# Kernel optimization log

Measured on AMD Instinct MI355X. Metric: run time of the kernel, lower is better.

## Reference

```python
import jax, jax.numpy as jnp
import numpy as np

EPS = 1e-5


def _bn(h, gamma, beta):
    # BatchNorm1d, training mode: biased batch statistics over nodes
    mu = jnp.mean(h, axis=0)
    var = jnp.mean(jnp.square(h - mu), axis=0)
    return (h - mu) * jax.lax.rsqrt(var + EPS) * gamma + beta


def setup_inputs() -> dict:
    key = jax.random.key(0)
    ks = jax.random.split(key, 12)
    N, E, D, H = 50000, 800000, 128, 256
    x = jax.random.normal(ks[0], (N, D), dtype=jnp.float32)
    edge_index = jax.random.randint(ks[1], (2, E), 0, N, dtype=jnp.int64)
    train_node_id = jax.random.randint(ks[2], (10000,), 0, N, dtype=jnp.int64)
    def lin(k, fan_in, fan_out):
        bound = 1.0 / np.sqrt(fan_in)
        return jax.random.uniform(k, (fan_in, fan_out), jnp.float32, -bound, bound)
    return {
        "x": x, "edge_index": edge_index, "train_node_id": train_node_id,
        "W1": lin(ks[3], D, H), "b1": jnp.zeros((H,), jnp.float32),
        "W2": lin(ks[4], H, H), "b2": jnp.zeros((H,), jnp.float32),
        "W3": lin(ks[5], H, H), "b3": jnp.zeros((H,), jnp.float32),
        "g1": jnp.ones((H,), jnp.float32), "be1": jnp.zeros((H,), jnp.float32),
        "g2": jnp.ones((H,), jnp.float32), "be2": jnp.zeros((H,), jnp.float32),
        "g3": jnp.ones((H,), jnp.float32), "be3": jnp.zeros((H,), jnp.float32),
        "Wl": lin(ks[6], H, H), "bl": jnp.zeros((H,), jnp.float32),
        "Wf": lin(ks[7], H, 1), "bf": jnp.zeros((1,), jnp.float32),
    }


def reference(x, edge_index, train_node_id, W1, b1, W2, b2, W3, b3,
              g1, be1, g2, be2, g3, be3, Wl, bl, Wf, bf):
    N = x.shape[0]
    loops = jnp.arange(N, dtype=edge_index.dtype)
    row = jnp.concatenate([edge_index[0], loops])  # destinations
    col = jnp.concatenate([edge_index[1], loops])  # sources
    deg = jax.ops.segment_sum(jnp.ones_like(row, dtype=x.dtype), row, num_segments=N)
    d_isqrt = jax.lax.rsqrt(deg)  # deg >= 1 due to self loops
    norm = (d_isqrt[row] * d_isqrt[col])[:, None]  # [E+N, 1]

    def gcn(h, W, b):
        hW = h @ W
        agg = jax.ops.segment_sum(hW[col] * norm, row, num_segments=N)
        return agg + b

    h = jax.nn.relu(_bn(gcn(x, W1, b1), g1, be1))
    h = jax.nn.relu(_bn(gcn(h, W2, b2), g2, be2))
    h = jax.nn.relu(_bn(gcn(h, W3, b3), g3, be3))
    h = jax.nn.relu(h @ Wl + bl)
    h = h[train_node_id]
    return jnp.squeeze(h @ Wf + bf, -1)
```

## Files before the change

### kernel.cpp

```cpp
#include <hip/hip_runtime.h>

typedef unsigned short u16;
typedef __attribute__((ext_vector_type(8))) short short8;
typedef __attribute__((ext_vector_type(4))) float f32x4;

#define CAP 96
#define GPB 25

#define DEVFN static __device__ __forceinline__

DEVFN float b2f(u16 u) {
    union { float f; unsigned v; } x; x.v = ((unsigned)u) << 16; return x.f;
}
DEVFN u16 f2b(float f) {
    union { float f; unsigned v; } x; x.f = f;
    unsigned r = x.v + 0x7fffu + ((x.v >> 16) & 1u);
    return (u16)(r >> 16);
}

DEVFN int detect64(const int* __restrict__ p) {
    int orv = 0;
#pragma unroll
    for (int i = 1; i < 64; i += 2) orv |= p[i];
    return (orv == 0) ? 1 : 0;
}

DEVFN void accum_row8(short8 v, float* acc) {
    const unsigned* u = (const unsigned*)&v;
#pragma unroll
    for (int k = 0; k < 4; k++) {
        union { float f; unsigned w; } lo, hi;
        lo.w = u[k] << 16;
        hi.w = u[k] & 0xffff0000u;
        acc[2 * k] += lo.f;
        acc[2 * k + 1] += hi.f;
    }
}

__global__ void k_init(const float* __restrict__ W1, const float* __restrict__ W2,
                       const float* __restrict__ W3, const float* __restrict__ Wl,
                       u16* __restrict__ T1, u16* __restrict__ T2,
                       u16* __restrict__ T3, u16* __restrict__ Tl,
                       int* __restrict__ ssrc, float* __restrict__ stat,
                       float* __restrict__ out, int N, int M) {
    int t = blockIdx.x * 256 + threadIdx.x;
    if (t < 229376) {
        const float* W; u16* T; int K; int idx;
        if (t < 32768)        { W = W1; T = T1; K = 128; idx = t; }
        else if (t < 98304)   { W = W2; T = T2; K = 256; idx = t - 32768; }
        else if (t < 163840)  { W = W3; T = T3; K = 256; idx = t - 98304; }
        else                  { W = Wl; T = Tl; K = 256; idx = t - 163840; }
        int k = idx >> 8, n = idx & 255;
        T[(size_t)n * K + k] = f2b(W[(size_t)k * 256 + n]);
    } else if (t < 229376 + 50000) {
        ssrc[(size_t)(t - 229376) * CAP] = 0;
    } else if (t < 229376 + 50000 + 1536) {
        stat[t - 229376 - 50000] = 0.0f;
    } else if (t < 229376 + 50000 + 1536 + 10000) {
        out[t - 229376 - 50000 - 1536] = 0.0f;
    }
}

__global__ void k_fillb(const int* __restrict__ ei, int* __restrict__ ssrc, int E) {
    int fl = detect64(ei);
    int t = blockIdx.x * 256 + threadIdx.x;
    int e0 = t * 2;
    if (e0 >= E) return;
    int r0, r1, c0, c1;
    bool two = (e0 + 1 < E);
    if (fl) {
        const int4* p4 = (const int4*)ei;
        int4 d = p4[t];
        int4 s = p4[(E >> 1) + t];
        r0 = d.x; r1 = d.z; c0 = s.x; c1 = s.z;
    } else {
        const int2* p2 = (const int2*)ei;
        int2 d = p2[t];
        int2 s = p2[(E >> 1) + t];
        r0 = d.x; r1 = d.y; c0 = s.x; c1 = s.y;
    }
    int p0 = atomicAdd(&ssrc[(size_t)r0 * CAP], 1);
    if (p0 < CAP - 1) ssrc[(size_t)r0 * CAP + 1 + p0] = c0;
    if (two) {
        int p1 = atomicAdd(&ssrc[(size_t)r1 * CAP], 1);
        if (p1 < CAP - 1) ssrc[(size_t)r1 * CAP + 1 + p1] = c1;
    }
}

__global__ void k_cvtx(const float* __restrict__ x, const int* __restrict__ ssrc,
                       float* __restrict__ disq, u16* __restrict__ xb, int n) {
    int i = (blockIdx.x * 256 + threadIdx.x) * 4;
    if (i >= n) return;
    int row = i >> 7;
    float d = rsqrtf((float)(ssrc[(size_t)row * CAP] + 1));
    if ((i & 127) == 0) disq[row] = d;
    float4 v = *(const float4*)(x + i);
    ushort4 o;
    o.x = f2b(v.x * d); o.y = f2b(v.y * d); o.z = f2b(v.z * d); o.w = f2b(v.w * d);
    *(ushort4*)(xb + i) = o;
}


template<int KS>
__global__ __launch_bounds__(256, 2) void k_gemm_rb(
        const u16* __restrict__ A, const u16* __restrict__ Wt,
        float* __restrict__ Cf, const int* __restrict__ idx,
        int Gtot, float* __restrict__ stat, const float* __restrict__ bias,
        const float* __restrict__ Wfp, const float* __restrict__ bfp,
        float* __restrict__ outp) {
    constexpr int K = KS * 32;
    __shared__ float sbuf[4][2][64];
    int wv = threadIdx.x >> 6;
    int lane = threadIdx.x & 63;
    int quad = lane >> 4;
    int mr = lane & 15;
    int colbase = blockIdx.y * 64;
    int g0 = blockIdx.x * GPB;

    short8 Bf[4][KS];
#pragma unroll
    for (int j = 0; j < 4; j++)
#pragma unroll
        for (int s = 0; s < KS; s++)
            Bf[j][s] = *(const short8*)(Wt + (size_t)(colbase + j * 16 + mr) * K + s * 32 + quad * 8);

    float4 bv4[4], wf4[4];
    if (Wfp) {
#pragma unroll
        for (int j = 0; j < 4; j++) {
            bv4[j] = *(const float4*)(bias + colbase + j * 16 + quad * 4);
            wf4[j] = *(const float4*)(Wfp + colbase + j * 16 + quad * 4);
        }
    }

    f32x4 sreg[4], s2reg[4];
#pragma unroll
    for (int j = 0; j < 4; j++) {
        sreg[j] = (f32x4){0.f, 0.f, 0.f, 0.f};
        s2reg[j] = (f32x4){0.f, 0.f, 0.f, 0.f};
    }
    int f = idx ? detect64(idx) : 0;

    for (int g = wv; g < GPB; g += 4) {
        int gg = g0 + g;
        if (gg >= Gtot) continue;
        int row = gg * 16 + mr;
        int arow = idx ? idx[(size_t)row << f] : row;
        const u16* Ap = A + (size_t)arow * K + quad * 8;

        short8 Af[KS];
#pragma unroll
        for (int s = 0; s < KS; s++) Af[s] = *(const short8*)(Ap + s * 32);

        f32x4 acc[4];
#pragma unroll
        for (int j = 0; j < 4; j++) acc[j] = (f32x4){0.f, 0.f, 0.f, 0.f};
#pragma unroll
        for (int s = 0; s < KS; s++)
#pragma unroll
            for (int j = 0; j < 4; j++)
                acc[j] = __builtin_amdgcn_mfma_f32_16x16x32_bf16(Bf[j][s], Af[s], acc[j], 0, 0, 0);

        if (Wfp) {
            float pr = 0.f;
#pragma unroll
            for (int j = 0; j < 4; j++) {
                const float* bj = (const float*)&bv4[j];
                const float* wj = (const float*)&wf4[j];
#pragma unroll
                for (int r = 0; r < 4; r++) {
                    float v = fmaxf(acc[j][r] + bj[r], 0.f);
                    pr += v * wj[r];
                }
            }
            pr += __shfl_xor(pr, 16, 64);
            pr += __shfl_xor(pr, 32, 64);
            if (quad == 0) {
                float v = pr;
                if (blockIdx.y == 0) v += bfp[0];
                atomicAdd(&outp[row], v);
            }
            continue;
        }

        float* cp = Cf + (size_t)row * 256 + colbase + quad * 4;
#pragma unroll
        for (int j = 0; j < 4; j++) {
            *(f32x4*)(cp + j * 16) = acc[j];
            sreg[j] += acc[j];
            s2reg[j] += acc[j] * acc[j];
        }
    }

    if (stat) {
#pragma unroll
        for (int j = 0; j < 4; j++) {
#pragma unroll
            for (int r = 0; r < 4; r++) {
                float a = sreg[j][r], b = s2reg[j][r];
                a += __shfl_xor(a, 1, 64); b += __shfl_xor(b, 1, 64);
                a += __shfl_xor(a, 2, 64); b += __shfl_xor(b, 2, 64);
                a += __shfl_xor(a, 4, 64); b += __shfl_xor(b, 4, 64);
                a += __shfl_xor(a, 8, 64); b += __shfl_xor(b, 8, 64);
                if (mr == 0) {
                    sbuf[wv][0][j * 16 + quad * 4 + r] = a;
                    sbuf[wv][1][j * 16 + quad * 4 + r] = b;
                }
            }
        }
        __syncthreads();
        int t = threadIdx.x;
        if (t < 128) {
            int which = t >> 6, c = t & 63;
            float v = sbuf[0][which][c] + sbuf[1][which][c] +
                      sbuf[2][which][c] + sbuf[3][which][c];
            atomicAdd(&stat[which * 256 + colbase + c], v);
        }
    }
}


__global__ __launch_bounds__(256) void k_gather256(
        const u16* __restrict__ src, const int* __restrict__ ssrc,
        const float* __restrict__ disq, u16* __restrict__ dst, int N) {
    int wave = threadIdx.x >> 6;
    int lane = threadIdx.x & 63;
    int half = lane >> 5;
    int l5 = lane & 31;
    int i = blockIdx.x * 4 + wave;
    if (i >= N) return;
    const u16* base = src + l5 * 8;
    const int* sp = ssrc + (size_t)i * CAP;
    float acc[8] = {0.f, 0.f, 0.f, 0.f, 0.f, 0.f, 0.f, 0.f};
    int e = min(sp[0], CAP - 1);
    int p = 0;
    for (; p + 8 <= e; p += 8) {
        int c0 = sp[1 + p + half];
        int c1 = sp[1 + p + 2 + half];
        int c2 = sp[1 + p + 4 + half];
        int c3 = sp[1 + p + 6 + half];
        short8 v0 = *(const short8*)(base + (size_t)c0 * 256);
        short8 v1 = *(const short8*)(base + (size_t)c1 * 256);
        short8 v2 = *(const short8*)(base + (size_t)c2 * 256);
        short8 v3 = *(const short8*)(base + (size_t)c3 * 256);
        accum_row8(v0, acc);
        accum_row8(v1, acc);
        accum_row8(v2, acc);
        accum_row8(v3, acc);
    }
    for (; p + 2 <= e; p += 2) {
        int c = sp[1 + p + half];
        short8 v = *(const short8*)(base + (size_t)c * 256);
        accum_row8(v, acc);
    }
    {
        int c = half ? i : ((p < e) ? sp[1 + p] : -1);
        if (c >= 0) {
            short8 v = *(const short8*)(base + (size_t)c * 256);
            accum_row8(v, acc);
        }
    }
#pragma unroll
    for (int k = 0; k < 8; k++) acc[k] += __shfl_xor(acc[k], 32, 64);
    if (half == 0) {
        float di = disq[i];
        short8 o;
        u16* op = (u16*)&o;
#pragma unroll
        for (int k = 0; k < 8; k++) op[k] = f2b(acc[k] * di);
        *(short8*)(dst + (size_t)i * 256 + l5 * 8) = o;
    }
}

__global__ __launch_bounds__(256) void k_gather128(
        const u16* __restrict__ src, const int* __restrict__ ssrc,
        const float* __restrict__ disq, u16* __restrict__ dst, int N) {
    int wave = threadIdx.x >> 6;
    int lane = threadIdx.x & 63;
    int q = lane >> 4;
    int l4 = lane & 15;
    int i = blockIdx.x * 4 + wave;
    if (i >= N) return;
    const u16* base = src + l4 * 8;
    const int* sp = ssrc + (size_t)i * CAP;
    float acc[8] = {0.f, 0.f, 0.f, 0.f, 0.f, 0.f, 0.f, 0.f};
    int e = min(sp[0], CAP - 1);
    int p = 0;
    for (; p + 8 <= e; p += 8) {
        int c0 = sp[1 + p + q];
        int c1 = sp[1 + p + 4 + q];
        short8 v0 = *(const short8*)(base + (size_t)c0 * 128);
        short8 v1 = *(const short8*)(base + (size_t)c1 * 128);
        accum_row8(v0, acc);
        accum_row8(v1, acc);
    }
    for (; p + 4 <= e; p += 4) {
        int c = sp[1 + p + q];
        short8 v = *(const short8*)(base + (size_t)c * 128);
        accum_row8(v, acc);
    }
    int rem = e - p;
    {
        int c = (q < rem) ? sp[1 + p + q] : ((q == 3) ? i : -1);
        if (c >= 0) {
            short8 v = *(const short8*)(base + (size_t)c * 128);
            accum_row8(v, acc);
        }
    }
#pragma unroll
    for (int k = 0; k < 8; k++) {
        acc[k] += __shfl_xor(acc[k], 16, 64);
        acc[k] += __shfl_xor(acc[k], 32, 64);
    }
    if (q == 0) {
        float di = disq[i];
        short8 o;
        u16* op = (u16*)&o;
#pragma unroll
        for (int k = 0; k < 8; k++) op[k] = f2b(acc[k] * di);
        *(short8*)(dst + (size_t)i * 128 + l4 * 8) = o;
    }
}


__global__ void k_bnapply(const float* __restrict__ t, const float* __restrict__ stat,
                          const float* __restrict__ gamma, const float* __restrict__ beta,
                          u16* __restrict__ h, int N, float invN,
                          const float* __restrict__ scale) {
    size_t tt = (size_t)blockIdx.x * 256 + threadIdx.x;
    size_t base = tt * 4;
    if (base >= (size_t)N * 256) return;
    int f0 = (int)(base & 255);
    float sc2 = scale ? scale[base >> 8] : 1.0f;
    float4 v = *(const float4*)(t + base);
    float r[4] = {v.x, v.y, v.z, v.w};
    ushort4 o;
    u16* op = (u16*)&o;
#pragma unroll
    for (int j = 0; j < 4; j++) {
        int f = f0 + j;
        float mean = stat[f] * invN;
        float var = stat[256 + f] * invN - mean * mean;
        float rstd = rsqrtf(var + 1e-5f);
        float sc = rstd * gamma[f];
        float sh = beta[f] - mean * sc;
        op[j] = f2b(fmaxf(r[j] * sc + sh, 0.0f) * sc2);
    }
    *(ushort4*)(h + base) = o;
}

__global__ void k_bnapply_idx(const float* __restrict__ t, const float* __restrict__ stat,
                              const float* __restrict__ gamma, const float* __restrict__ beta,
                              const int* __restrict__ idx, u16* __restrict__ zin,
                              int M, float invN) {
    int fl = detect64(idx);
    size_t tt = (size_t)blockIdx.x * 256 + threadIdx.x;
    size_t base = tt * 4;
    if (base >= (size_t)M * 256) return;
    int f0 = (int)(base & 255);
    int row = (int)(base >> 8);
    int node = idx[(size_t)row << fl];
    float4 v = *(const float4*)(t + (size_t)node * 256 + f0);
    float r[4] = {v.x, v.y, v.z, v.w};
    ushort4 o;
    u16* op = (u16*)&o;
#pragma unroll
    for (int j = 0; j < 4; j++) {
        int f = f0 + j;
        float mean = stat[f] * invN;
        float var = stat[256 + f] * invN - mean * mean;
        float rstd = rsqrtf(var + 1e-5f);
        float sc = rstd * gamma[f];
        float sh = beta[f] - mean * sc;
        op[j] = f2b(fmaxf(r[j] * sc + sh, 0.0f));
    }
    *(ushort4*)(zin + (size_t)row * 256 + f0) = o;
}


extern "C" void kernel_launch(void* const* d_in, const int* in_sizes, int n_in,
                              void* d_out, int out_size, void* d_ws, size_t ws_size,
                              hipStream_t stream) {
    const int D = 128, H = 256;
    const int N = in_sizes[0] / D;
    const int E = in_sizes[1] / 2;
    const int M = in_sizes[2];

    const float* x = (const float*)d_in[0];
    const int* ei = (const int*)d_in[1];
    const int* tnid = (const int*)d_in[2];
    const float* W1 = (const float*)d_in[3];
    const float* W2 = (const float*)d_in[5];
    const float* W3 = (const float*)d_in[7];
    const float* g1 = (const float*)d_in[9];
    const float* be1 = (const float*)d_in[10];
    const float* g2 = (const float*)d_in[11];
    const float* be2 = (const float*)d_in[12];
    const float* g3 = (const float*)d_in[13];
    const float* be3 = (const float*)d_in[14];
    const float* Wl = (const float*)d_in[15];
    const float* bl = (const float*)d_in[16];
    const float* Wf = (const float*)d_in[17];
    const float* bfp = (const float*)d_in[18];
    float* out = (float*)d_out;

    char* w = (char*)d_ws;
    size_t off = 0;
    auto carve = [&](size_t bytes) -> void* {
        void* p = w + off;
        off = (off + bytes + 255) & ~(size_t)255;
        return p;
    };

    float* stat = (float*)carve(3 * 512 * 4);
    float* disq = (float*)carve((size_t)N * 4);
    int* ssrc = (int*)carve((size_t)N * CAP * 4);
    u16* Wt1 = (u16*)carve((size_t)H * D * 2);
    u16* Wt2 = (u16*)carve((size_t)H * H * 2);
    u16* Wt3 = (u16*)carve((size_t)H * H * 2);
    u16* Wtl = (u16*)carve((size_t)H * H * 2);
    u16* xb = (u16*)carve((size_t)N * D * 2);
    u16* aggx = (u16*)carve((size_t)N * D * 2);
    u16* aggh = (u16*)carve((size_t)N * H * 2);
    float* tb = (float*)carve((size_t)N * H * 4);
    u16* hb = (u16*)carve((size_t)N * H * 2);
    u16* zin = (u16*)carve((size_t)M * H * 2);

    const float invN = 1.0f / (float)N;

    const int Gn = N / 16;
    const int Gm = M / 16;
    dim3 gemm_grid((Gn + GPB - 1) / GPB, 4);
    dim3 gemm_grid_m((Gm + GPB - 1) / GPB, 4);
    const int AB = (N + 3) / 4;
    const int PB = (int)(((size_t)N * H / 4 + 255) / 256);
    const int PBm = (int)(((size_t)M * H / 4 + 255) / 256);

    k_init<<<(229376 + 50000 + 1536 + 10000 + 255) / 256, 256, 0, stream>>>(
        W1, W2, W3, Wl, Wt1, Wt2, Wt3, Wtl, ssrc, stat, out, N, M);
    k_fillb<<<(E / 2 + 255) / 256, 256, 0, stream>>>(ei, ssrc, E);
    k_cvtx<<<(N * D / 4 + 255) / 256, 256, 0, stream>>>(x, ssrc, disq, xb, N * D);

    k_gather128<<<AB, 256, 0, stream>>>(xb, ssrc, disq, aggx, N);
    k_gemm_rb<4><<<gemm_grid, 256, 0, stream>>>(aggx, Wt1, tb, nullptr, Gn, stat, nullptr, nullptr, nullptr, nullptr);
    k_bnapply<<<PB, 256, 0, stream>>>(tb, stat, g1, be1, hb, N, invN, disq);
    k_gather256<<<AB, 256, 0, stream>>>(hb, ssrc, disq, aggh, N);
    k_gemm_rb<8><<<gemm_grid, 256, 0, stream>>>(aggh, Wt2, tb, nullptr, Gn, stat + 512, nullptr, nullptr, nullptr, nullptr);
    k_bnapply<<<PB, 256, 0, stream>>>(tb, stat + 512, g2, be2, hb, N, invN, disq);
    k_gather256<<<AB, 256, 0, stream>>>(hb, ssrc, disq, aggh, N);
    k_gemm_rb<8><<<gemm_grid, 256, 0, stream>>>(aggh, Wt3, tb, nullptr, Gn, stat + 1024, nullptr, nullptr, nullptr, nullptr);
    k_bnapply_idx<<<PBm, 256, 0, stream>>>(tb, stat + 1024, g3, be3, tnid, zin, M, invN);

    k_gemm_rb<8><<<gemm_grid_m, 256, 0, stream>>>(zin, Wtl, nullptr, nullptr, Gm, nullptr, bl, Wf, bfp, out);
}
```

Before: 447.8 us.

## Store features in 32-column planes and gather per plane with u16 adjacency

Feature matrices now use a planar layout of 32-column slabs, so each gather block works on one plane and touches a smaller, more cache-resident source slice. Adjacency is stored as 16-bit source ids in a fixed 32-slot array plus an overflow array, which shrinks the index footprint. The GEMMs read A through a plane stride, and the gather loops over the maximum degree among the 16 nodes handled by each wave. Risks: 16-bit ids only hold node indices below 65536, neighbours beyond 95 per node are silently dropped, and lanes whose node has a lower degree sit idle for the extra iterations.

```diff
diff --git a/kernel.cpp b/kernel.cpp
--- a/kernel.cpp
+++ b/kernel.cpp
@@ -4,7 +4,6 @@
 typedef __attribute__((ext_vector_type(8))) short short8;
 typedef __attribute__((ext_vector_type(4))) float f32x4;
 
-#define CAP 96
 #define GPB 25
 
 #define DEVFN static __device__ __forceinline__
@@ -41,7 +40,7 @@
                        const float* __restrict__ W3, const float* __restrict__ Wl,
                        u16* __restrict__ T1, u16* __restrict__ T2,
                        u16* __restrict__ T3, u16* __restrict__ Tl,
-                       int* __restrict__ ssrc, float* __restrict__ stat,
+                       int* __restrict__ cnt, float* __restrict__ stat,
                        float* __restrict__ out, int N, int M) {
     int t = blockIdx.x * 256 + threadIdx.x;
     if (t < 229376) {
@@ -52,16 +51,17 @@
         else                  { W = Wl; T = Tl; K = 256; idx = t - 163840; }
         int k = idx >> 8, n = idx & 255;
         T[(size_t)n * K + k] = f2b(W[(size_t)k * 256 + n]);
-    } else if (t < 229376 + 50000) {
-        ssrc[(size_t)(t - 229376) * CAP] = 0;
-    } else if (t < 229376 + 50000 + 1536) {
-        stat[t - 229376 - 50000] = 0.0f;
-    } else if (t < 229376 + 50000 + 1536 + 10000) {
-        out[t - 229376 - 50000 - 1536] = 0.0f;
-    }
-}
-
-__global__ void k_fillb(const int* __restrict__ ei, int* __restrict__ ssrc, int E) {
+    } else if (t < 229376 + N) {
+        cnt[t - 229376] = 0;
+    } else if (t < 229376 + N + 1536) {
+        stat[t - 229376 - N] = 0.0f;
+    } else if (t < 229376 + N + 1536 + M) {
+        out[t - 229376 - N - 1536] = 0.0f;
+    }
+}
+
+__global__ void k_fillb(const int* __restrict__ ei, int* __restrict__ cnt,
+                        u16* __restrict__ slots, u16* __restrict__ ovf, int E) {
     int fl = detect64(ei);
     int t = blockIdx.x * 256 + threadIdx.x;
     int e0 = t * 2;
@@ -79,33 +79,98 @@
         int2 s = p2[(E >> 1) + t];
         r0 = d.x; r1 = d.y; c0 = s.x; c1 = s.y;
     }
-    int p0 = atomicAdd(&ssrc[(size_t)r0 * CAP], 1);
-    if (p0 < CAP - 1) ssrc[(size_t)r0 * CAP + 1 + p0] = c0;
+    int p0 = atomicAdd(&cnt[r0], 1);
+    if (p0 < 32)      slots[(size_t)r0 * 32 + p0] = (u16)c0;
+    else if (p0 < 96) ovf[(size_t)r0 * 64 + (p0 - 32)] = (u16)c0;
     if (two) {
-        int p1 = atomicAdd(&ssrc[(size_t)r1 * CAP], 1);
-        if (p1 < CAP - 1) ssrc[(size_t)r1 * CAP + 1 + p1] = c1;
-    }
-}
-
-__global__ void k_cvtx(const float* __restrict__ x, const int* __restrict__ ssrc,
-                       float* __restrict__ disq, u16* __restrict__ xb, int n) {
-    int i = (blockIdx.x * 256 + threadIdx.x) * 4;
-    if (i >= n) return;
-    int row = i >> 7;
-    float d = rsqrtf((float)(ssrc[(size_t)row * CAP] + 1));
-    if ((i & 127) == 0) disq[row] = d;
-    float4 v = *(const float4*)(x + i);
+        int p1 = atomicAdd(&cnt[r1], 1);
+        if (p1 < 32)      slots[(size_t)r1 * 32 + p1] = (u16)c1;
+        else if (p1 < 96) ovf[(size_t)r1 * 64 + (p1 - 32)] = (u16)c1;
+    }
+}
+
+__global__ void k_cvtx(const float* __restrict__ x, const int* __restrict__ cnt,
+                       float* __restrict__ disq, u16* __restrict__ xb, int N) {
+    int t = blockIdx.x * 256 + threadIdx.x;
+    if (t >= N * 32) return;
+    int row = t >> 5;
+    int f0 = (t & 31) * 4;
+    float d = rsqrtf((float)(cnt[row] + 1));
+    if ((t & 31) == 0) disq[row] = d;
+    float4 v = *(const float4*)(x + (size_t)row * 128 + f0);
     ushort4 o;
     o.x = f2b(v.x * d); o.y = f2b(v.y * d); o.z = f2b(v.z * d); o.w = f2b(v.w * d);
-    *(ushort4*)(xb + i) = o;
+    *(ushort4*)(xb + (size_t)(f0 >> 5) * N * 32 + (size_t)row * 32 + (f0 & 31)) = o;
+}
+
+
+template<int PBITS>
+__global__ __launch_bounds__(256) void k_gatherP(
+        const u16* __restrict__ src, const int* __restrict__ cnt,
+        const u16* __restrict__ slots, const u16* __restrict__ ovf,
+        const float* __restrict__ disq, u16* __restrict__ dst, int N) {
+    const int NP = 1 << PBITS;
+    const size_t N32 = (size_t)N * 32;
+    int plane = blockIdx.x & (NP - 1);
+    int lane = threadIdx.x & 63;
+    int wv = threadIdx.x >> 6;
+    int j = lane >> 2;
+    int piece = lane & 3;
+    int d = (blockIdx.x >> PBITS) * 64 + wv * 16 + j;
+    bool live = d < N;
+    int e = live ? min(cnt[d], 95) : -1;
+
+    const u16* sbase = src + (size_t)plane * N32 + piece * 8;
+    const u16* sl = slots + (size_t)d * 32;
+    const u16* ov = ovf + (size_t)d * 64;
+
+    float acc[8] = {0.f, 0.f, 0.f, 0.f, 0.f, 0.f, 0.f, 0.f};
+
+    int m = e;
+    m = max(m, __shfl_xor(m, 4, 64));
+    m = max(m, __shfl_xor(m, 8, 64));
+    m = max(m, __shfl_xor(m, 16, 64));
+    m = max(m, __shfl_xor(m, 32, 64));
+
+    int mm = min(m, 31);
+#pragma unroll 4
+    for (int r = 0; r <= mm; r++) {
+        int c = -1;
+        if (r < e) c = (int)sl[r];
+        else if (r == e) c = d;
+        if (c >= 0) {
+            short8 v = *(const short8*)(sbase + (size_t)c * 32);
+            accum_row8(v, acc);
+        }
+    }
+    if (m >= 32) {
+        for (int r = 32; r <= m; r++) {
+            int c = -1;
+            if (r < e) c = (int)ov[r - 32];
+            else if (r == e) c = d;
+            if (c >= 0) {
+                short8 v = *(const short8*)(sbase + (size_t)c * 32);
+                accum_row8(v, acc);
+            }
+        }
+    }
+    if (live) {
+        float di = disq[d];
+        short8 o;
+        u16* op = (u16*)&o;
+#pragma unroll
+        for (int k = 0; k < 8; k++) op[k] = f2b(acc[k] * di);
+        __builtin_nontemporal_store(o,
+            (short8*)(dst + (size_t)plane * N32 + (size_t)d * 32 + piece * 8));
+    }
 }
 
 
 template<int KS>
 __global__ __launch_bounds__(256, 2) void k_gemm_rb(
         const u16* __restrict__ A, const u16* __restrict__ Wt,
-        float* __restrict__ Cf, const int* __restrict__ idx,
-        int Gtot, float* __restrict__ stat, const float* __restrict__ bias,
+        float* __restrict__ Cf, int PS, int Gtot,
+        float* __restrict__ stat, const float* __restrict__ bias,
         const float* __restrict__ Wfp, const float* __restrict__ bfp,
         float* __restrict__ outp) {
     constexpr int K = KS * 32;
@@ -139,18 +204,16 @@
         sreg[j] = (f32x4){0.f, 0.f, 0.f, 0.f};
         s2reg[j] = (f32x4){0.f, 0.f, 0.f, 0.f};
     }
-    int f = idx ? detect64(idx) : 0;
 
     for (int g = wv; g < GPB; g += 4) {
         int gg = g0 + g;
         if (gg >= Gtot) continue;
         int row = gg * 16 + mr;
-        int arow = idx ? idx[(size_t)row << f] : row;
-        const u16* Ap = A + (size_t)arow * K + quad * 8;
+        const u16* Ap = A + (size_t)row * 32 + quad * 8;
 
         short8 Af[KS];
 #pragma unroll
-        for (int s = 0; s < KS; s++) Af[s] = *(const short8*)(Ap + s * 32);
+        for (int s = 0; s < KS; s++) Af[s] = *(const short8*)(Ap + (size_t)s * PS);
 
         f32x4 acc[4];
 #pragma unroll
@@ -220,109 +283,6 @@
 }
 
 
-__global__ __launch_bounds__(256) void k_gather256(
-        const u16* __restrict__ src, const int* __restrict__ ssrc,
-        const float* __restrict__ disq, u16* __restrict__ dst, int N) {
-    int wave = threadIdx.x >> 6;
-    int lane = threadIdx.x & 63;
-    int half = lane >> 5;
-    int l5 = lane & 31;
-    int i = blockIdx.x * 4 + wave;
-    if (i >= N) return;
-    const u16* base = src + l5 * 8;
-    const int* sp = ssrc + (size_t)i * CAP;
-    float acc[8] = {0.f, 0.f, 0.f, 0.f, 0.f, 0.f, 0.f, 0.f};
-    int e = min(sp[0], CAP - 1);
-    int p = 0;
-    for (; p + 8 <= e; p += 8) {
-        int c0 = sp[1 + p + half];
-        int c1 = sp[1 + p + 2 + half];
-        int c2 = sp[1 + p + 4 + half];
-        int c3 = sp[1 + p + 6 + half];
-        short8 v0 = *(const short8*)(base + (size_t)c0 * 256);
-        short8 v1 = *(const short8*)(base + (size_t)c1 * 256);
-        short8 v2 = *(const short8*)(base + (size_t)c2 * 256);
-        short8 v3 = *(const short8*)(base + (size_t)c3 * 256);
-        accum_row8(v0, acc);
-        accum_row8(v1, acc);
-        accum_row8(v2, acc);
-        accum_row8(v3, acc);
-    }
-    for (; p + 2 <= e; p += 2) {
-        int c = sp[1 + p + half];
-        short8 v = *(const short8*)(base + (size_t)c * 256);
-        accum_row8(v, acc);
-    }
-    {
-        int c = half ? i : ((p < e) ? sp[1 + p] : -1);
-        if (c >= 0) {
-            short8 v = *(const short8*)(base + (size_t)c * 256);
-            accum_row8(v, acc);
-        }
-    }
-#pragma unroll
-    for (int k = 0; k < 8; k++) acc[k] += __shfl_xor(acc[k], 32, 64);
-    if (half == 0) {
-        float di = disq[i];
-        short8 o;
-        u16* op = (u16*)&o;
-#pragma unroll
-        for (int k = 0; k < 8; k++) op[k] = f2b(acc[k] * di);
-        *(short8*)(dst + (size_t)i * 256 + l5 * 8) = o;
-    }
-}
-
-__global__ __launch_bounds__(256) void k_gather128(
-        const u16* __restrict__ src, const int* __restrict__ ssrc,
-        const float* __restrict__ disq, u16* __restrict__ dst, int N) {
-    int wave = threadIdx.x >> 6;
-    int lane = threadIdx.x & 63;
-    int q = lane >> 4;
-    int l4 = lane & 15;
-    int i = blockIdx.x * 4 + wave;
-    if (i >= N) return;
-    const u16* base = src + l4 * 8;
-    const int* sp = ssrc + (size_t)i * CAP;
-    float acc[8] = {0.f, 0.f, 0.f, 0.f, 0.f, 0.f, 0.f, 0.f};
-    int e = min(sp[0], CAP - 1);
-    int p = 0;
-    for (; p + 8 <= e; p += 8) {
-        int c0 = sp[1 + p + q];
-        int c1 = sp[1 + p + 4 + q];
-        short8 v0 = *(const short8*)(base + (size_t)c0 * 128);
-        short8 v1 = *(const short8*)(base + (size_t)c1 * 128);
-        accum_row8(v0, acc);
-        accum_row8(v1, acc);
-    }
-    for (; p + 4 <= e; p += 4) {
-        int c = sp[1 + p + q];
-        short8 v = *(const short8*)(base + (size_t)c * 128);
-        accum_row8(v, acc);
-    }
-    int rem = e - p;
-    {
-        int c = (q < rem) ? sp[1 + p + q] : ((q == 3) ? i : -1);
-        if (c >= 0) {
-            short8 v = *(const short8*)(base + (size_t)c * 128);
-            accum_row8(v, acc);
-        }
-    }
-#pragma unroll
-    for (int k = 0; k < 8; k++) {
-        acc[k] += __shfl_xor(acc[k], 16, 64);
-        acc[k] += __shfl_xor(acc[k], 32, 64);
-    }
-    if (q == 0) {
-        float di = disq[i];
-        short8 o;
-        u16* op = (u16*)&o;
-#pragma unroll
-        for (int k = 0; k < 8; k++) op[k] = f2b(acc[k] * di);
-        *(short8*)(dst + (size_t)i * 128 + l4 * 8) = o;
-    }
-}
-
-
 __global__ void k_bnapply(const float* __restrict__ t, const float* __restrict__ stat,
                           const float* __restrict__ gamma, const float* __restrict__ beta,
                           u16* __restrict__ h, int N, float invN,
@@ -331,7 +291,8 @@
     size_t base = tt * 4;
     if (base >= (size_t)N * 256) return;
     int f0 = (int)(base & 255);
-    float sc2 = scale ? scale[base >> 8] : 1.0f;
+    int row = (int)(base >> 8);
+    float sc2 = scale ? scale[row] : 1.0f;
     float4 v = *(const float4*)(t + base);
     float r[4] = {v.x, v.y, v.z, v.w};
     ushort4 o;
@@ -346,7 +307,7 @@
         float sh = beta[f] - mean * sc;
         op[j] = f2b(fmaxf(r[j] * sc + sh, 0.0f) * sc2);
     }
-    *(ushort4*)(h + base) = o;
+    *(ushort4*)(h + (size_t)(f0 >> 5) * N * 32 + (size_t)row * 32 + (f0 & 31)) = o;
 }
 
 __global__ void k_bnapply_idx(const float* __restrict__ t, const float* __restrict__ stat,
@@ -374,7 +335,7 @@
         float sh = beta[f] - mean * sc;
         op[j] = f2b(fmaxf(r[j] * sc + sh, 0.0f));
     }
-    *(ushort4*)(zin + (size_t)row * 256 + f0) = o;
+    *(ushort4*)(zin + (size_t)(f0 >> 5) * M * 32 + (size_t)row * 32 + (f0 & 31)) = o;
 }
 
 
@@ -414,7 +375,9 @@
 
     float* stat = (float*)carve(3 * 512 * 4);
     float* disq = (float*)carve((size_t)N * 4);
-    int* ssrc = (int*)carve((size_t)N * CAP * 4);
+    int* cnt = (int*)carve((size_t)N * 4);
+    u16* slots = (u16*)carve((size_t)N * 32 * 2);
+    u16* ovf = (u16*)carve((size_t)N * 64 * 2);
     u16* Wt1 = (u16*)carve((size_t)H * D * 2);
     u16* Wt2 = (u16*)carve((size_t)H * H * 2);
     u16* Wt3 = (u16*)carve((size_t)H * H * 2);
@@ -432,24 +395,26 @@
     const int Gm = M / 16;
     dim3 gemm_grid((Gn + GPB - 1) / GPB, 4);
     dim3 gemm_grid_m((Gm + GPB - 1) / GPB, 4);
-    const int AB = (N + 3) / 4;
+    const int PSn = N * 32;
+    const int PSm = M * 32;
+    const int chunks = (N + 63) / 64;
     const int PB = (int)(((size_t)N * H / 4 + 255) / 256);
     const int PBm = (int)(((size_t)M * H / 4 + 255) / 256);
 
-    k_init<<<(229376 + 50000 + 1536 + 10000 + 255) / 256, 256, 0, stream>>>(
-        W1, W2, W3, Wl, Wt1, Wt2, Wt3, Wtl, ssrc, stat, out, N, M);
-    k_fillb<<<(E / 2 + 255) / 256, 256, 0, stream>>>(ei, ssrc, E);
-    k_cvtx<<<(N * D / 4 + 255) / 256, 256, 0, stream>>>(x, ssrc, disq, xb, N * D);
-
-    k_gather128<<<AB, 256, 0, stream>>>(xb, ssrc, disq, aggx, N);
-    k_gemm_rb<4><<<gemm_grid, 256, 0, stream>>>(aggx, Wt1, tb, nullptr, Gn, stat, nullptr, nullptr, nullptr, nullptr);
+    k_init<<<(229376 + N + 1536 + M + 255) / 256, 256, 0, stream>>>(
+        W1, W2, W3, Wl, Wt1, Wt2, Wt3, Wtl, cnt, stat, out, N, M);
+    k_fillb<<<(E / 2 + 255) / 256, 256, 0, stream>>>(ei, cnt, slots, ovf, E);
+    k_cvtx<<<(N * 32 + 255) / 256, 256, 0, stream>>>(x, cnt, disq, xb, N);
+
+    k_gatherP<2><<<4 * chunks, 256, 0, stream>>>(xb, cnt, slots, ovf, disq, aggx, N);
+    k_gemm_rb<4><<<gemm_grid, 256, 0, stream>>>(aggx, Wt1, tb, PSn, Gn, stat, nullptr, nullptr, nullptr, nullptr);
     k_bnapply<<<PB, 256, 0, stream>>>(tb, stat, g1, be1, hb, N, invN, disq);
-    k_gather256<<<AB, 256, 0, stream>>>(hb, ssrc, disq, aggh, N);
-    k_gemm_rb<8><<<gemm_grid, 256, 0, stream>>>(aggh, Wt2, tb, nullptr, Gn, stat + 512, nullptr, nullptr, nullptr, nullptr);
+    k_gatherP<3><<<8 * chunks, 256, 0, stream>>>(hb, cnt, slots, ovf, disq, aggh, N);
+    k_gemm_rb<8><<<gemm_grid, 256, 0, stream>>>(aggh, Wt2, tb, PSn, Gn, stat + 512, nullptr, nullptr, nullptr, nullptr);
     k_bnapply<<<PB, 256, 0, stream>>>(tb, stat + 512, g2, be2, hb, N, invN, disq);
-    k_gather256<<<AB, 256, 0, stream>>>(hb, ssrc, disq, aggh, N);
-    k_gemm_rb<8><<<gemm_grid, 256, 0, stream>>>(aggh, Wt3, tb, nullptr, Gn, stat + 1024, nullptr, nullptr, nullptr, nullptr);
+    k_gatherP<3><<<8 * chunks, 256, 0, stream>>>(hb, cnt, slots, ovf, disq, aggh, N);
+    k_gemm_rb<8><<<gemm_grid, 256, 0, stream>>>(aggh, Wt3, tb, PSn, Gn, stat + 1024, nullptr, nullptr, nullptr, nullptr);
     k_bnapply_idx<<<PBm, 256, 0, stream>>>(tb, stat + 1024, g3, be3, tnid, zin, M, invN);
 
-    k_gemm_rb<8><<<gemm_grid_m, 256, 0, stream>>>(zin, Wtl, nullptr, nullptr, Gm, nullptr, bl, Wf, bfp, out);
-}
+    k_gemm_rb<8><<<gemm_grid_m, 256, 0, stream>>>(zin, Wtl, nullptr, PSm, Gm, nullptr, bl, Wf, bfp, out);
+}
```

New measurement: 489.8 us. 9.4% more time.
